# Kernel tuning notes

Hardware: AMD Instinct MI355X
Metric: run time of the kernel (lower is better)

Reference implementation:

```python
import jax, jax.numpy as jnp
import numpy as np

H = 128  # hidden/input size fixed by module


def setup_inputs() -> dict:
    key = jax.random.key(0)
    ks = jax.random.split(key, 8)
    S, B = 512, 256
    scale = 1.0 / np.sqrt(H)
    return {
        "X": jax.random.normal(ks[0], (S, B, H), dtype=jnp.float32),
        "h": jax.random.normal(ks[1], (1, B, H), dtype=jnp.float32),
        "lin_W": jax.random.uniform(ks[2], (H, H), jnp.float32, -scale, scale),
        "lin_b": jax.random.uniform(ks[3], (H,), jnp.float32, -scale, scale),
        "W_ih": jax.random.uniform(ks[4], (3 * H, H), jnp.float32, -scale, scale),
        "W_hh": jax.random.uniform(ks[5], (3 * H, H), jnp.float32, -scale, scale),
        "b_ih": jax.random.uniform(ks[6], (3 * H,), jnp.float32, -scale, scale),
        "b_hh": jax.random.uniform(ks[7], (3 * H,), jnp.float32, -scale, scale),
    }


def reference(X, h, lin_W, lin_b, W_ih, W_hh, b_ih, b_hh):
    # Linear: y = X @ W^T + b   (torch nn.Linear convention)
    Xp = jnp.einsum("sbd,ed->sbe", X, lin_W) + lin_b
    # Precompute input-hidden gate projections for all timesteps: (S, B, 3H)
    gx_all = jnp.einsum("sbd,gd->sbg", Xp, W_ih) + b_ih

    def step(h_t, gx):
        gh = h_t @ W_hh.T + b_hh  # (B, 3H)
        xr, xz, xn = jnp.split(gx, 3, axis=-1)
        hr, hz, hn = jnp.split(gh, 3, axis=-1)
        r = jax.nn.sigmoid(xr + hr)
        z = jax.nn.sigmoid(xz + hz)
        n = jnp.tanh(xn + r * hn)
        h_new = (1.0 - z) * n + z * h_t
        return h_new, h_new

    _, outs = jax.lax.scan(step, h[0], gx_all)
    return outs  # (S, B, H) — the module returns only the output sequence
```

## Files before the change

### kernel.cpp

```cpp
#include <hip/hip_runtime.h>
#include <math.h>

#define HID 128
#define G3  384
#define BATCH 256
#define SEQ 512
#define NB 16
#define NBLK (BATCH/NB)

typedef __bf16 bf16x8 __attribute__((ext_vector_type(8)));
typedef __bf16 bf16x4 __attribute__((ext_vector_type(4)));
typedef float  f32x4  __attribute__((ext_vector_type(4)));

#define LOG2E 1.44269504088896f

__device__ __forceinline__ float sigm(float x) {
    return __builtin_amdgcn_rcpf(1.f + __builtin_amdgcn_exp2f(-LOG2E * x));
}
__device__ __forceinline__ float tanh_fast(float x) {
    float e = __builtin_amdgcn_exp2f(-2.f * LOG2E * x);
    return __builtin_amdgcn_rcpf(1.f + e) * 2.f - 1.f;
}
__device__ __forceinline__ f32x4 mfma16(bf16x8 a, bf16x8 b, f32x4 c) {
    return __builtin_amdgcn_mfma_f32_16x16x32_bf16(a, b, c, 0, 0, 0);
}
__device__ __forceinline__ bf16x8 cvt8(float4 a, float4 b) {
    bf16x8 f;
    f[0] = (__bf16)a.x; f[1] = (__bf16)a.y; f[2] = (__bf16)a.z; f[3] = (__bf16)a.w;
    f[4] = (__bf16)b.x; f[5] = (__bf16)b.y; f[6] = (__bf16)b.z; f[7] = (__bf16)b.w;
    return f;
}
__device__ __forceinline__ bf16x4 cvt4(float4 a) {
    bf16x4 f;
    f[0] = (__bf16)a.x; f[1] = (__bf16)a.y; f[2] = (__bf16)a.z; f[3] = (__bf16)a.w;
    return f;
}

__global__ void fold_kernel(const float* __restrict__ lin_W,
                            const float* __restrict__ lin_b,
                            const float* __restrict__ W_ih,
                            const float* __restrict__ b_ih,
                            float* __restrict__ Wc,
                            float* __restrict__ bcA) {
    const int g = blockIdx.x;
    const int d = threadIdx.x;
    float acc = 0.f;
    for (int e = 0; e < HID; ++e) acc += W_ih[g * HID + e] * lin_W[e * HID + d];
    Wc[g * HID + d] = acc;
    if (d == 0) {
        float b = 0.f;
        for (int e = 0; e < HID; ++e) b += W_ih[g * HID + e] * lin_b[e];
        bcA[g] = b + b_ih[g];
    }
}

__global__ __launch_bounds__(512, 2)
void gru_scan_mfma(const float* __restrict__ X,
                   const float* __restrict__ h0,
                   const float* __restrict__ W_hh,
                   const float* __restrict__ b_hh,
                   const float* __restrict__ Wc,
                   const float* __restrict__ bcA,
                   float* __restrict__ out) {
    const int t   = threadIdx.x;
    const int w   = t >> 6;
    const int l   = t & 63;
    const int col = l & 15;
    const int lr  = l >> 4;
    const int bb  = blockIdx.x * NB;

    __shared__ __align__(16) unsigned char lds[16384];
    unsigned char* hA = lds;
    unsigned char* hB = lds + 4096;
    unsigned char* xA = lds + 8192;
    unsigned char* xB = lds + 12288;

    auto SW = [](int b, int off) { return b * 256 + (off ^ ((b & 7) << 4)); };

    bf16x8 aW[3][4], aC[3][4];
    #pragma unroll
    for (int g3 = 0; g3 < 3; ++g3)
        #pragma unroll
        for (int kt = 0; kt < 4; ++kt) {
            const int row = g3 * HID + w * 16 + col;
            const float* pw = W_hh + row * HID + kt * 32 + lr * 8;
            const float* pc = Wc   + row * HID + kt * 32 + lr * 8;
            aW[g3][kt] = cvt8(*(const float4*)pw, *(const float4*)(pw + 4));
            aC[g3][kt] = cvt8(*(const float4*)pc, *(const float4*)(pc + 4));
        }
    #pragma unroll
    for (int g3 = 0; g3 < 3; ++g3)
        #pragma unroll
        for (int kt = 0; kt < 4; ++kt) {
            asm volatile("" : "+v"(aW[g3][kt]));
            asm volatile("" : "+v"(aC[g3][kt]));
        }

    f32x4 vbr, vbz, vbnx, vbnh;
    #pragma unroll
    for (int q = 0; q < 4; ++q) {
        const int g = w * 16 + lr * 4 + q;
        vbr[q]  = bcA[g] + b_hh[g];
        vbz[q]  = bcA[HID + g] + b_hh[HID + g];
        vbnx[q] = bcA[2 * HID + g];
        vbnh[q] = b_hh[2 * HID + g];
    }

    f32x4 hold = *(const f32x4*)(h0 + (size_t)(bb + col) * HID + w * 16 + lr * 4);

    const int sb = t >> 5;
    const int sk = (t & 31) * 4;

    float4 xp, xq;
    if (t < 256) {
        const int hb = t >> 4, hk = (t & 15) * 8;
        const float* ph = h0 + (size_t)(bb + hb) * HID + hk;
        *(bf16x8*)(hA + SW(hb, hk * 2)) =
            cvt8(*(const float4*)ph, *(const float4*)(ph + 4));
    }
    {
        const float* px = X + ((size_t)0 * BATCH + bb + sb) * HID + sk;
        *(bf16x4*)(xA + SW(sb, sk * 2)) = cvt4(*(const float4*)px);
        const float* p1 = X + ((size_t)1 * BATCH + bb + sb) * HID + sk;
        xp = *(const float4*)p1;
    }
    asm volatile("s_waitcnt lgkmcnt(0)" ::: "memory");
    __builtin_amdgcn_s_barrier();

    auto STEP = [&](int s, unsigned char* hR, unsigned char* hW,
                    unsigned char* xR, unsigned char* xW,
                    float4& xc, float4& xn) {
        *(bf16x4*)(xW + SW(sb, sk * 2)) = cvt4(xc);

        {
            int sp = s + 2; if (sp > SEQ - 1) sp = SEQ - 1;
            const float* px = X + ((size_t)sp * BATCH + bb + sb) * HID + sk;
            xn = *(const float4*)px;
        }

        bf16x8 Bh[4], Bx[4];
        #pragma unroll
        for (int kt = 0; kt < 4; ++kt) {
            Bh[kt] = *(const bf16x8*)(hR + SW(col, kt * 64 + lr * 16));
            Bx[kt] = *(const bf16x8*)(xR + SW(col, kt * 64 + lr * 16));
        }

        f32x4 ar = vbr, az = vbz, anh = vbnh, anx = vbnx;
        #pragma unroll
        for (int kt = 0; kt < 4; ++kt) {
            ar  = mfma16(aW[0][kt], Bh[kt], ar);
            ar  = mfma16(aC[0][kt], Bx[kt], ar);
            az  = mfma16(aW[1][kt], Bh[kt], az);
            az  = mfma16(aC[1][kt], Bx[kt], az);
            anh = mfma16(aW[2][kt], Bh[kt], anh);
            anx = mfma16(aC[2][kt], Bx[kt], anx);
        }

        f32x4 hnew;
        #pragma unroll
        for (int q = 0; q < 4; ++q) {
            float r = sigm(ar[q]);
            float z = sigm(az[q]);
            float n = tanh_fast(anx[q] + r * anh[q]);
            hnew[q] = n + z * (hold[q] - n);
        }
        hold = hnew;
        *(bf16x4*)(hW + SW(col, (w * 16 + lr * 4) * 2)) = cvt4(*(float4*)&hnew);
        float4 o; o.x = hnew[0]; o.y = hnew[1]; o.z = hnew[2]; o.w = hnew[3];
        *(float4*)(out + ((size_t)s * BATCH + bb + col) * HID + w * 16 + lr * 4) = o;

        asm volatile("s_waitcnt lgkmcnt(0)" ::: "memory");
        __builtin_amdgcn_s_barrier();
    };

    for (int s0 = 0; s0 < SEQ; s0 += 2) {
        STEP(s0,     hA, hB, xA, xB, xp, xq);
        STEP(s0 + 1, hB, hA, xB, xA, xq, xp);
    }
}

extern "C" void kernel_launch(void* const* d_in, const int* in_sizes, int n_in,
                              void* d_out, int out_size, void* d_ws, size_t ws_size,
                              hipStream_t stream) {
    const float* X     = (const float*)d_in[0];
    const float* h0    = (const float*)d_in[1];
    const float* lin_W = (const float*)d_in[2];
    const float* lin_b = (const float*)d_in[3];
    const float* W_ih  = (const float*)d_in[4];
    const float* W_hh  = (const float*)d_in[5];
    const float* b_ih  = (const float*)d_in[6];
    const float* b_hh  = (const float*)d_in[7];
    float* out = (float*)d_out;

    float* Wc  = (float*)d_ws;
    float* bcA = Wc + G3 * HID;

    fold_kernel<<<G3, HID, 0, stream>>>(lin_W, lin_b, W_ih, b_ih, Wc, bcA);
    gru_scan_mfma<<<NBLK, 512, 0, stream>>>(X, h0, W_hh, b_hh, Wc, bcA, out);
}
```

Before: 439.1 us.

## Precompute input gate projections in a parallel GEMM before the GRU scan

Adds a bf16 MFMA GEMM kernel that computes the folded input projections for all timesteps into a workspace buffer. A lighter scan kernel then only does the recurrent W_hh MFMAs and reads the precomputed gates with a one-step prefetch. This halves the serial per-step matrix work and removes X staging through LDS. In exchange it writes and reads a large bf16 intermediate, adds a kernel launch, and stores gate inputs in bf16. It falls back to the old path if the workspace is too small.

```diff
diff --git a/kernel.cpp b/kernel.cpp
--- a/kernel.cpp
+++ b/kernel.cpp
@@ -34,6 +34,177 @@
     bf16x4 f;
     f[0] = (__bf16)a.x; f[1] = (__bf16)a.y; f[2] = (__bf16)a.z; f[3] = (__bf16)a.w;
     return f;
+}
+__device__ __forceinline__ float bflo(unsigned u) { return __uint_as_float(u << 16); }
+__device__ __forceinline__ float bfhi(unsigned u) { return __uint_as_float(u & 0xffff0000u); }
+
+
+__global__ void fold_bf16_kernel(const float* __restrict__ lin_W,
+                                 const float* __restrict__ lin_b,
+                                 const float* __restrict__ W_ih,
+                                 const float* __restrict__ b_ih,
+                                 __bf16* __restrict__ Wcbf,
+                                 float* __restrict__ bcA) {
+    const int g = blockIdx.x;
+    const int d = threadIdx.x;
+    float acc = 0.f;
+    for (int e = 0; e < HID; ++e) acc += W_ih[g * HID + e] * lin_W[e * HID + d];
+    Wcbf[g * HID + d] = (__bf16)acc;
+    if (d == 0) {
+        float b = 0.f;
+        for (int e = 0; e < HID; ++e) b += W_ih[g * HID + e] * lin_b[e];
+        bcA[g] = b + b_ih[g];
+    }
+}
+
+__global__ __launch_bounds__(512, 2)
+void gemm_gx_kernel(const float* __restrict__ X,
+                    const __bf16* __restrict__ Wcbf,
+                    const float* __restrict__ bcA,
+                    __bf16* __restrict__ gx) {
+    const int t   = threadIdx.x;
+    const int w   = t >> 6;
+    const int l   = t & 63;
+    const int col = l & 15;
+    const int lr  = l >> 4;
+    const int m   = blockIdx.x * 128 + w * 16 + col;
+
+    bf16x8 Bx[4];
+    const float* px = X + (size_t)m * HID + lr * 8;
+    #pragma unroll
+    for (int kt = 0; kt < 4; ++kt)
+        Bx[kt] = cvt8(*(const float4*)(px + kt * 32), *(const float4*)(px + kt * 32 + 4));
+
+    #pragma unroll 4
+    for (int gt = 0; gt < 24; ++gt) {
+        const int g0 = gt * 16;
+        const __bf16* pa = Wcbf + (size_t)(g0 + col) * HID + lr * 8;
+        bf16x8 A0 = *(const bf16x8*)(pa);
+        bf16x8 A1 = *(const bf16x8*)(pa + 32);
+        bf16x8 A2 = *(const bf16x8*)(pa + 64);
+        bf16x8 A3 = *(const bf16x8*)(pa + 96);
+        float4 bc4 = *(const float4*)(bcA + g0 + lr * 4);
+        f32x4 acc; acc[0] = bc4.x; acc[1] = bc4.y; acc[2] = bc4.z; acc[3] = bc4.w;
+        acc = mfma16(A0, Bx[0], acc);
+        acc = mfma16(A1, Bx[1], acc);
+        acc = mfma16(A2, Bx[2], acc);
+        acc = mfma16(A3, Bx[3], acc);
+        float4 o; o.x = acc[0]; o.y = acc[1]; o.z = acc[2]; o.w = acc[3];
+        *(bf16x4*)(gx + (size_t)m * G3 + g0 + lr * 4) = cvt4(o);
+    }
+}
+
+__global__ __launch_bounds__(512, 2)
+void gru_scan_light(const float* __restrict__ h0,
+                    const float* __restrict__ W_hh,
+                    const float* __restrict__ b_hh,
+                    const __bf16* __restrict__ gx,
+                    float* __restrict__ out) {
+    const int t   = threadIdx.x;
+    const int w   = t >> 6;
+    const int l   = t & 63;
+    const int col = l & 15;
+    const int lr  = l >> 4;
+    const int bb  = blockIdx.x * NB;
+
+    __shared__ __align__(16) unsigned char lds[8192];
+    unsigned char* hA = lds;
+    unsigned char* hB = lds + 4096;
+
+    auto SW = [](int b, int off) { return b * 256 + (off ^ ((b & 7) << 4)); };
+
+    bf16x8 aW[3][4];
+    #pragma unroll
+    for (int g3 = 0; g3 < 3; ++g3)
+        #pragma unroll
+        for (int kt = 0; kt < 4; ++kt) {
+            const int row = g3 * HID + w * 16 + col;
+            const float* pw = W_hh + row * HID + kt * 32 + lr * 8;
+            aW[g3][kt] = cvt8(*(const float4*)pw, *(const float4*)(pw + 4));
+        }
+    #pragma unroll
+    for (int g3 = 0; g3 < 3; ++g3)
+        #pragma unroll
+        for (int kt = 0; kt < 4; ++kt)
+            asm volatile("" : "+v"(aW[g3][kt]));
+
+    f32x4 vbr, vbz, vbnh;
+    #pragma unroll
+    for (int q = 0; q < 4; ++q) {
+        const int g = w * 16 + lr * 4 + q;
+        vbr[q]  = b_hh[g];
+        vbz[q]  = b_hh[HID + g];
+        vbnh[q] = b_hh[2 * HID + g];
+    }
+
+    f32x4 hold = *(const f32x4*)(h0 + (size_t)(bb + col) * HID + w * 16 + lr * 4);
+
+    const size_t gxoff = (size_t)(bb + col) * G3 + w * 16 + lr * 4;
+
+    if (t < 256) {
+        const int hb = t >> 4, hk = (t & 15) * 8;
+        const float* ph = h0 + (size_t)(bb + hb) * HID + hk;
+        *(bf16x8*)(hA + SW(hb, hk * 2)) =
+            cvt8(*(const float4*)ph, *(const float4*)(ph + 4));
+    }
+    uint2 gpr, gpz, gpn, gqr, gqz, gqn;
+    {
+        const __bf16* p = gx + gxoff;
+        gpr = *(const uint2*)(p);
+        gpz = *(const uint2*)(p + HID);
+        gpn = *(const uint2*)(p + 2 * HID);
+    }
+    asm volatile("s_waitcnt lgkmcnt(0)" ::: "memory");
+    __builtin_amdgcn_s_barrier();
+
+    auto STEP = [&](int s, unsigned char* hR, unsigned char* hW,
+                    uint2& gcr, uint2& gcz, uint2& gcn,
+                    uint2& gnr, uint2& gnz, uint2& gnn) {
+        {
+            int sp = s + 1; if (sp > SEQ - 1) sp = SEQ - 1;
+            const __bf16* p = gx + (size_t)sp * BATCH * G3 + gxoff;
+            gnr = *(const uint2*)(p);
+            gnz = *(const uint2*)(p + HID);
+            gnn = *(const uint2*)(p + 2 * HID);
+        }
+
+        bf16x8 Bh[4];
+        #pragma unroll
+        for (int kt = 0; kt < 4; ++kt)
+            Bh[kt] = *(const bf16x8*)(hR + SW(col, kt * 64 + lr * 16));
+
+        f32x4 ar = vbr, az = vbz, anh = vbnh;
+        #pragma unroll
+        for (int kt = 0; kt < 4; ++kt) {
+            ar  = mfma16(aW[0][kt], Bh[kt], ar);
+            az  = mfma16(aW[1][kt], Bh[kt], az);
+            anh = mfma16(aW[2][kt], Bh[kt], anh);
+        }
+
+        float xr[4] = { bflo(gcr.x), bfhi(gcr.x), bflo(gcr.y), bfhi(gcr.y) };
+        float xz[4] = { bflo(gcz.x), bfhi(gcz.x), bflo(gcz.y), bfhi(gcz.y) };
+        float xn[4] = { bflo(gcn.x), bfhi(gcn.x), bflo(gcn.y), bfhi(gcn.y) };
+        f32x4 hnew;
+        #pragma unroll
+        for (int q = 0; q < 4; ++q) {
+            float r = sigm(ar[q] + xr[q]);
+            float z = sigm(az[q] + xz[q]);
+            float n = tanh_fast(xn[q] + r * anh[q]);
+            hnew[q] = n + z * (hold[q] - n);
+        }
+        hold = hnew;
+        *(bf16x4*)(hW + SW(col, (w * 16 + lr * 4) * 2)) = cvt4(*(float4*)&hnew);
+        float4 o; o.x = hnew[0]; o.y = hnew[1]; o.z = hnew[2]; o.w = hnew[3];
+        *(float4*)(out + ((size_t)s * BATCH + bb + col) * HID + w * 16 + lr * 4) = o;
+
+        asm volatile("s_waitcnt lgkmcnt(0)" ::: "memory");
+        __builtin_amdgcn_s_barrier();
+    };
+
+    for (int s0 = 0; s0 < SEQ; s0 += 2) {
+        STEP(s0,     hA, hB, gpr, gpz, gpn, gqr, gqz, gqn);
+        STEP(s0 + 1, hB, hA, gqr, gqz, gqn, gpr, gpz, gpn);
+    }
 }
 
 __global__ void fold_kernel(const float* __restrict__ lin_W,
@@ -131,20 +302,17 @@
                     unsigned char* xR, unsigned char* xW,
                     float4& xc, float4& xn) {
         *(bf16x4*)(xW + SW(sb, sk * 2)) = cvt4(xc);
-
         {
             int sp = s + 2; if (sp > SEQ - 1) sp = SEQ - 1;
             const float* px = X + ((size_t)sp * BATCH + bb + sb) * HID + sk;
             xn = *(const float4*)px;
         }
-
         bf16x8 Bh[4], Bx[4];
         #pragma unroll
         for (int kt = 0; kt < 4; ++kt) {
             Bh[kt] = *(const bf16x8*)(hR + SW(col, kt * 64 + lr * 16));
             Bx[kt] = *(const bf16x8*)(xR + SW(col, kt * 64 + lr * 16));
         }
-
         f32x4 ar = vbr, az = vbz, anh = vbnh, anx = vbnx;
         #pragma unroll
         for (int kt = 0; kt < 4; ++kt) {
@@ -155,7 +323,6 @@
             anh = mfma16(aW[2][kt], Bh[kt], anh);
             anx = mfma16(aC[2][kt], Bx[kt], anx);
         }
-
         f32x4 hnew;
         #pragma unroll
         for (int q = 0; q < 4; ++q) {
@@ -168,7 +335,6 @@
         *(bf16x4*)(hW + SW(col, (w * 16 + lr * 4) * 2)) = cvt4(*(float4*)&hnew);
         float4 o; o.x = hnew[0]; o.y = hnew[1]; o.z = hnew[2]; o.w = hnew[3];
         *(float4*)(out + ((size_t)s * BATCH + bb + col) * HID + w * 16 + lr * 4) = o;
-
         asm volatile("s_waitcnt lgkmcnt(0)" ::: "memory");
         __builtin_amdgcn_s_barrier();
     };
@@ -192,9 +358,22 @@
     const float* b_hh  = (const float*)d_in[7];
     float* out = (float*)d_out;
 
-    float* Wc  = (float*)d_ws;
-    float* bcA = Wc + G3 * HID;
-
-    fold_kernel<<<G3, HID, 0, stream>>>(lin_W, lin_b, W_ih, b_ih, Wc, bcA);
-    gru_scan_mfma<<<NBLK, 512, 0, stream>>>(X, h0, W_hh, b_hh, Wc, bcA, out);
-}
+    const size_t GX_BYTES   = (size_t)SEQ * BATCH * G3 * 2;
+    const size_t WCBF_BYTES = (size_t)G3 * HID * 2;
+    const size_t BCA_BYTES  = (size_t)G3 * 4;
+
+    if (ws_size >= GX_BYTES + WCBF_BYTES + BCA_BYTES) {
+        __bf16* gxp  = (__bf16*)d_ws;
+        __bf16* Wcbf = (__bf16*)((char*)d_ws + GX_BYTES);
+        float*  bcA  = (float*)((char*)d_ws + GX_BYTES + WCBF_BYTES);
+
+        fold_bf16_kernel<<<G3, HID, 0, stream>>>(lin_W, lin_b, W_ih, b_ih, Wcbf, bcA);
+        gemm_gx_kernel<<<(SEQ * BATCH) / 128, 512, 0, stream>>>(X, Wcbf, bcA, gxp);
+        gru_scan_light<<<NBLK, 512, 0, stream>>>(h0, W_hh, b_hh, gxp, out);
+    } else {
+        float* Wc  = (float*)d_ws;
+        float* bcA = Wc + G3 * HID;
+        fold_kernel<<<G3, HID, 0, stream>>>(lin_W, lin_b, W_ih, b_ih, Wc, bcA);
+        gru_scan_mfma<<<NBLK, 512, 0, stream>>>(X, h0, W_hh, b_hh, Wc, bcA, out);
+    }
+}
```

New measurement: 513.4 us. 1.17x slower.
